# Optimization experiments

Measured on AMD Instinct MI355X. Metric: run time of the kernel, lower is better.

The kernel has to match this reference:

```python
import jax, jax.numpy as jnp
import numpy as np

B, N, DIM, DD = 32, 4096, 512, 512
SCALE = DD ** -0.5


def setup_inputs() -> dict:
    key = jax.random.key(0)
    ks = jax.random.split(key, 7)
    return {
        "x": jax.random.normal(ks[0], (B, N, DIM), dtype=jnp.float32),
        "Wq": jax.random.normal(ks[1], (DIM, DD), dtype=jnp.float32) * (DIM ** -0.5),
        "Wk": jax.random.normal(ks[2], (DIM, DD), dtype=jnp.float32) * (DIM ** -0.5),
        "Wv": jax.random.normal(ks[3], (DIM, DD), dtype=jnp.float32) * (DIM ** -0.5),
        "Wr": jax.random.normal(ks[4], (DD, DD), dtype=jnp.float32) * (DD ** -0.5),
        "alpha": jax.random.normal(ks[5], (DD,), dtype=jnp.float32),
        "beta": jax.random.normal(ks[6], (DD,), dtype=jnp.float32),
    }


def reference(x, Wq, Wk, Wv, Wr, alpha, beta):
    # projections: [b, n, d]
    q = jnp.einsum('bni,id->bnd', x, Wq)
    k = jnp.einsum('bni,id->bnd', x, Wk)
    v = jnp.einsum('bni,id->bnd', x, Wv)
    # additive attention over feature dim, pooled over sequence
    alpha_w = jax.nn.softmax(q * alpha * SCALE, axis=-1)
    global_query = jnp.sum(q * alpha_w, axis=1)            # [b, d]
    p = global_query[:, None, :] * k                        # [b, n, d]
    beta_w = jax.nn.softmax(p * beta * SCALE, axis=-1)
    global_key = jnp.sum(p * beta_w, axis=1)                # [b, d]
    kv = global_key[:, None, :] * v                         # [b, n, d]
    out = jnp.einsum('bnd,de->bne', kv, Wr) + q
    return out
```

## Files before the change

kernel.cpp:

```cpp
#include <hip/hip_runtime.h>


typedef __attribute__((ext_vector_type(8))) short short8;
typedef __attribute__((ext_vector_type(4))) float floatx4;
typedef unsigned short u16;
typedef unsigned int u32;

#define SEQ 4096
#define BATCH 32
#define NQKV 1536
#define FSCALE 0.044194173824159216f

__device__ __forceinline__ u16 f2bf(float f) {
  u32 u = __float_as_uint(f);
  u += 0x7fffu + ((u >> 16) & 1u);
  return (u16)(u >> 16);
}
__device__ __forceinline__ float bf2f(u16 h) { return __uint_as_float((u32)h << 16); }

__device__ __forceinline__ void g2l16(const void* g, void* l) {
  __builtin_amdgcn_global_load_lds(
      (const __attribute__((address_space(1))) void*)g,
      (__attribute__((address_space(3))) void*)l, 16, 0, 0);
}

__global__ __launch_bounds__(256) void convert_x(const float* __restrict__ x,
                                                 u16* __restrict__ xb) {
  size_t i = ((size_t)blockIdx.x * 256 + threadIdx.x) * 8;
  float4 f0 = *(const float4*)(x + i);
  float4 f1 = *(const float4*)(x + i + 4);
  short8 s;
  s[0] = (short)f2bf(f0.x); s[1] = (short)f2bf(f0.y);
  s[2] = (short)f2bf(f0.z); s[3] = (short)f2bf(f0.w);
  s[4] = (short)f2bf(f1.x); s[5] = (short)f2bf(f1.y);
  s[6] = (short)f2bf(f1.z); s[7] = (short)f2bf(f1.w);
  *(short8*)(xb + i) = s;
}

__global__ void prep_w(const float* __restrict__ Wq, const float* __restrict__ Wk,
                       const float* __restrict__ Wv, u16* __restrict__ Wt) {
  int n = blockIdx.x;
  const float* W = (n < 512) ? Wq : ((n < 1024) ? Wk : Wv);
  int col = n & 511;
  for (int kk = threadIdx.x; kk < 512; kk += 256)
    Wt[(size_t)n * 512 + kk] = f2bf(W[(size_t)kk * 512 + col]);
}

__global__ __launch_bounds__(256) void gemm_qkv(const u16* __restrict__ xb,
                                                const u16* __restrict__ Wt,
                                                u16* __restrict__ qkv) {
  __shared__ u16 sA[128 * 32];
  __shared__ u16 sB[128 * 32];
  const int tid = threadIdx.x;
  const int lane = tid & 63, wv = tid >> 6;
  const int row0 = blockIdx.y * 128;
  const int col0 = blockIdx.x * 128;
  const int wm = (wv >> 1) * 64, wn = (wv & 1) * 64;

  floatx4 acc[4][4] = {};
  const int ln = lane & 15;
  const int quad = (lane >> 4);
  const int b_row = (lane >> 2);
  const int b_kq = (lane & 3) * 8;

  for (int kt = 0; kt < 16; ++kt) {
    const int k0 = kt * 32;
    __syncthreads();
#pragma unroll
    for (int c = 0; c < 2; ++c) {
      int chunk = wv * 2 + c;
      int r = chunk * 16 + b_row;
      g2l16(xb + (size_t)(row0 + r) * 512 + k0 + b_kq, sA + chunk * 512 + lane * 8);
      g2l16(Wt + (size_t)(col0 + r) * 512 + k0 + b_kq, sB + chunk * 512 + lane * 8);
    }
    __syncthreads();

    short8 a[4], b[4];
#pragma unroll
    for (int i = 0; i < 4; ++i)
      a[i] = *(const short8*)&sA[(wm + i * 16 + ln) * 32 + quad * 8];
#pragma unroll
    for (int j = 0; j < 4; ++j)
      b[j] = *(const short8*)&sB[(wn + j * 16 + ln) * 32 + quad * 8];
#pragma unroll
    for (int i = 0; i < 4; ++i)
#pragma unroll
      for (int j = 0; j < 4; ++j)
        acc[i][j] = __builtin_amdgcn_mfma_f32_16x16x32_bf16(a[i], b[j], acc[i][j], 0, 0, 0);
  }

#pragma unroll
  for (int i = 0; i < 4; ++i) {
#pragma unroll
    for (int r = 0; r < 4; ++r) {
      int grow = row0 + wm + i * 16 + quad * 4 + r;
      size_t base = (size_t)grow * NQKV + col0 + wn + ln;
#pragma unroll
      for (int j = 0; j < 4; ++j)
        qkv[base + j * 16] = f2bf(acc[i][j][r]);
    }
  }
}

__global__ __launch_bounds__(256) void pool_alpha(const u16* __restrict__ qkv,
                                                  const float* __restrict__ alpha,
                                                  float* __restrict__ gq) {
  const int b = blockIdx.y;
  const int lane = threadIdx.x & 63, wv = threadIdx.x >> 6;
  const int slot = blockIdx.x * 4 + wv;
  float a8[8], acc8[8];
#pragma unroll
  for (int j = 0; j < 8; ++j) {
    a8[j] = alpha[lane * 8 + j] * FSCALE;
    acc8[j] = 0.f;
  }
  for (int i = 0; i < 64; ++i) {
    int row = slot * 64 + i;
    const u16* qr = qkv + (size_t)(b * SEQ + row) * NQKV + lane * 8;
    short8 s = *(const short8*)qr;
    float q[8], t[8];
    float m = -1e30f;
#pragma unroll
    for (int j = 0; j < 8; ++j) {
      q[j] = bf2f((u16)s[j]);
      t[j] = q[j] * a8[j];
      m = fmaxf(m, t[j]);
    }
#pragma unroll
    for (int off = 32; off >= 1; off >>= 1) m = fmaxf(m, __shfl_xor(m, off));
    float sum = 0.f;
    float e[8];
#pragma unroll
    for (int j = 0; j < 8; ++j) {
      e[j] = __expf(t[j] - m);
      sum += e[j];
    }
#pragma unroll
    for (int off = 32; off >= 1; off >>= 1) sum += __shfl_xor(sum, off);
    float inv = 1.f / sum;
#pragma unroll
    for (int j = 0; j < 8; ++j) acc8[j] += q[j] * e[j] * inv;
  }
#pragma unroll
  for (int j = 0; j < 8; ++j) atomicAdd(&gq[b * 512 + lane * 8 + j], acc8[j]);
}

__global__ __launch_bounds__(256) void pool_beta(const u16* __restrict__ qkv,
                                                 const float* __restrict__ beta,
                                                 const float* __restrict__ gq,
                                                 float* __restrict__ gk) {
  const int b = blockIdx.y;
  const int lane = threadIdx.x & 63, wv = threadIdx.x >> 6;
  const int slot = blockIdx.x * 4 + wv;
  float b8[8], g8[8], acc8[8];
#pragma unroll
  for (int j = 0; j < 8; ++j) {
    b8[j] = beta[lane * 8 + j] * FSCALE;
    g8[j] = gq[b * 512 + lane * 8 + j];
    acc8[j] = 0.f;
  }
  for (int i = 0; i < 64; ++i) {
    int row = slot * 64 + i;
    const u16* kr = qkv + (size_t)(b * SEQ + row) * NQKV + 512 + lane * 8;
    short8 s = *(const short8*)kr;
    float p[8], t[8];
    float m = -1e30f;
#pragma unroll
    for (int j = 0; j < 8; ++j) {
      p[j] = g8[j] * bf2f((u16)s[j]);
      t[j] = p[j] * b8[j];
      m = fmaxf(m, t[j]);
    }
#pragma unroll
    for (int off = 32; off >= 1; off >>= 1) m = fmaxf(m, __shfl_xor(m, off));
    float sum = 0.f;
    float e[8];
#pragma unroll
    for (int j = 0; j < 8; ++j) {
      e[j] = __expf(t[j] - m);
      sum += e[j];
    }
#pragma unroll
    for (int off = 32; off >= 1; off >>= 1) sum += __shfl_xor(sum, off);
    float inv = 1.f / sum;
#pragma unroll
    for (int j = 0; j < 8; ++j) acc8[j] += p[j] * e[j] * inv;
  }
#pragma unroll
  for (int j = 0; j < 8; ++j) atomicAdd(&gk[b * 512 + lane * 8 + j], acc8[j]);
}

__global__ void build_wrs(const float* __restrict__ Wr, const float* __restrict__ gk,
                          u16* __restrict__ Wrs) {
  int e = blockIdx.x, b = blockIdx.y;
  const float* g = gk + b * 512;
  u16* o = Wrs + ((size_t)b * 512 + e) * 512;
  for (int d = threadIdx.x; d < 512; d += 256)
    o[d] = f2bf(g[d] * Wr[(size_t)d * 512 + e]);
}

__global__ __launch_bounds__(256) void gemm_out(const u16* __restrict__ qkv,
                                                const u16* __restrict__ Wrs,
                                                float* __restrict__ out) {
  __shared__ u16 sA[128 * 32];
  __shared__ u16 sB[128 * 32];
  const int tid = threadIdx.x;
  const int lane = tid & 63, wv = tid >> 6;
  const int b = blockIdx.z;
  const int row0 = blockIdx.y * 128;
  const int col0 = blockIdx.x * 128;
  const int wm = (wv >> 1) * 64, wn = (wv & 1) * 64;

  floatx4 acc[4][4] = {};
  const int ln = lane & 15;
  const int quad = (lane >> 4);
  const int b_row = (lane >> 2);
  const int b_kq = (lane & 3) * 8;

  const u16* vbase = qkv + (size_t)b * SEQ * NQKV + 1024;
  const u16* wbase = Wrs + (size_t)b * 512 * 512;

  for (int kt = 0; kt < 16; ++kt) {
    const int k0 = kt * 32;
    __syncthreads();
#pragma unroll
    for (int c = 0; c < 2; ++c) {
      int chunk = wv * 2 + c;
      int r = chunk * 16 + b_row;
      g2l16(vbase + (size_t)(row0 + r) * NQKV + k0 + b_kq, sA + chunk * 512 + lane * 8);
      g2l16(wbase + (size_t)(col0 + r) * 512 + k0 + b_kq, sB + chunk * 512 + lane * 8);
    }
    __syncthreads();

    short8 a[4], bb[4];
#pragma unroll
    for (int i = 0; i < 4; ++i)
      a[i] = *(const short8*)&sA[(wm + i * 16 + ln) * 32 + quad * 8];
#pragma unroll
    for (int j = 0; j < 4; ++j)
      bb[j] = *(const short8*)&sB[(wn + j * 16 + ln) * 32 + quad * 8];
#pragma unroll
    for (int i = 0; i < 4; ++i)
#pragma unroll
      for (int j = 0; j < 4; ++j)
        acc[i][j] = __builtin_amdgcn_mfma_f32_16x16x32_bf16(a[i], bb[j], acc[i][j], 0, 0, 0);
  }

#pragma unroll
  for (int i = 0; i < 4; ++i) {
#pragma unroll
    for (int r = 0; r < 4; ++r) {
      int grow = row0 + wm + i * 16 + quad * 4 + r;
      size_t qrow = (size_t)(b * SEQ + grow) * NQKV;
      size_t orow = (size_t)(b * SEQ + grow) * 512;
#pragma unroll
      for (int j = 0; j < 4; ++j) {
        int gcol = col0 + wn + ln + j * 16;
        float qv = bf2f(qkv[qrow + gcol]);
        out[orow + gcol] = acc[i][j][r] + qv;
      }
    }
  }
}

extern "C" void kernel_launch(void* const* d_in, const int* in_sizes, int n_in,
                              void* d_out, int out_size, void* d_ws, size_t ws_size,
                              hipStream_t stream) {
  const float* x = (const float*)d_in[0];
  const float* Wq = (const float*)d_in[1];
  const float* Wk = (const float*)d_in[2];
  const float* Wv = (const float*)d_in[3];
  const float* Wr = (const float*)d_in[4];
  const float* alpha = (const float*)d_in[5];
  const float* beta = (const float*)d_in[6];
  float* out = (float*)d_out;

  char* ws = (char*)d_ws;
  u16* qkv = (u16*)ws;
  u16* Wt = (u16*)(ws + 402653184ull);
  u16* Wrs = (u16*)(ws + 402653184ull + 1572864ull);
  float* gq = (float*)(ws + 402653184ull + 1572864ull + 16777216ull);
  float* gk = gq + 16384;

  u16* xb = (u16*)d_out;

  hipMemsetAsync(gq, 0, 131072, stream);
  convert_x<<<32768, 256, 0, stream>>>(x, xb);
  prep_w<<<1536, 256, 0, stream>>>(Wq, Wk, Wv, Wt);
  gemm_qkv<<<dim3(12, 1024), 256, 0, stream>>>(xb, Wt, qkv);
  pool_alpha<<<dim3(16, BATCH), 256, 0, stream>>>(qkv, alpha, gq);
  pool_beta<<<dim3(16, BATCH), 256, 0, stream>>>(qkv, beta, gq, gk);
  build_wrs<<<dim3(512, BATCH), 256, 0, stream>>>(Wr, gk, Wrs);
  gemm_out<<<dim3(4, 32, BATCH), 256, 0, stream>>>(qkv, Wrs, out);
}
```

Measured before the change: 1.163 ms.

## Fold V projection, gk scaling, Wr and Q residual into per-batch output weight

Instead of computing V and then multiplying by a gk-scaled Wr, the output is rewritten as x times a per-batch fused matrix Wv·diag(gk)·Wr + Wq. That matrix is built with a small batched GEMM, and the final GEMM then reads x directly. This drops the V columns from the big projection GEMM and removes the separate residual read of q in the epilogue. It also adds a grouped block-index swizzle to the large GEMMs for cache locality. In exchange, Wq is now rounded to bf16 inside the fused weight, which changes numerics slightly, and the residual q is recomputed through the fused weight rather than reused.

```diff
diff --git a/kernel.cpp b/kernel.cpp
--- a/kernel.cpp
+++ b/kernel.cpp
@@ -8,7 +8,7 @@
 
 #define SEQ 4096
 #define BATCH 32
-#define NQKV 1536
+#define NQK 1024
 #define FSCALE 0.044194173824159216f
 
 __device__ __forceinline__ u16 f2bf(float f) {
@@ -38,40 +38,44 @@
 }
 
 __global__ void prep_w(const float* __restrict__ Wq, const float* __restrict__ Wk,
-                       const float* __restrict__ Wv, u16* __restrict__ Wt) {
+                       const float* __restrict__ Wr, u16* __restrict__ Wt,
+                       u16* __restrict__ Wrt) {
   int n = blockIdx.x;
-  const float* W = (n < 512) ? Wq : ((n < 1024) ? Wk : Wv);
-  int col = n & 511;
-  for (int kk = threadIdx.x; kk < 512; kk += 256)
-    Wt[(size_t)n * 512 + kk] = f2bf(W[(size_t)kk * 512 + col]);
-}
-
-__global__ __launch_bounds__(256) void gemm_qkv(const u16* __restrict__ xb,
-                                                const u16* __restrict__ Wt,
-                                                u16* __restrict__ qkv) {
-  __shared__ u16 sA[128 * 32];
-  __shared__ u16 sB[128 * 32];
+  if (n < 1024) {
+    const float* W = (n < 512) ? Wq : Wk;
+    int col = n & 511;
+    for (int kk = threadIdx.x; kk < 512; kk += 256)
+      Wt[(size_t)n * 512 + kk] = f2bf(W[(size_t)kk * 512 + col]);
+  } else {
+    int e = n - 1024;
+    for (int d = threadIdx.x; d < 512; d += 256)
+      Wrt[(size_t)e * 512 + d] = f2bf(Wr[(size_t)d * 512 + e]);
+  }
+}
+
+template <int LDA, int LDB, int KTILES>
+__device__ __forceinline__ void gemm_core(const u16* __restrict__ A,
+                                          const u16* __restrict__ B,
+                                          int row0, int col0,
+                                          u16* sA, u16* sB,
+                                          floatx4 (&acc)[4][4]) {
   const int tid = threadIdx.x;
   const int lane = tid & 63, wv = tid >> 6;
-  const int row0 = blockIdx.y * 128;
-  const int col0 = blockIdx.x * 128;
   const int wm = (wv >> 1) * 64, wn = (wv & 1) * 64;
-
-  floatx4 acc[4][4] = {};
   const int ln = lane & 15;
-  const int quad = (lane >> 4);
-  const int b_row = (lane >> 2);
+  const int quad = lane >> 4;
+  const int b_row = lane >> 2;
   const int b_kq = (lane & 3) * 8;
 
-  for (int kt = 0; kt < 16; ++kt) {
+  for (int kt = 0; kt < KTILES; ++kt) {
     const int k0 = kt * 32;
     __syncthreads();
 #pragma unroll
     for (int c = 0; c < 2; ++c) {
       int chunk = wv * 2 + c;
       int r = chunk * 16 + b_row;
-      g2l16(xb + (size_t)(row0 + r) * 512 + k0 + b_kq, sA + chunk * 512 + lane * 8);
-      g2l16(Wt + (size_t)(col0 + r) * 512 + k0 + b_kq, sB + chunk * 512 + lane * 8);
+      g2l16(A + (size_t)(row0 + r) * LDA + k0 + b_kq, sA + chunk * 512 + lane * 8);
+      g2l16(B + (size_t)(col0 + r) * LDB + k0 + b_kq, sB + chunk * 512 + lane * 8);
     }
     __syncthreads();
 
@@ -88,21 +92,37 @@
       for (int j = 0; j < 4; ++j)
         acc[i][j] = __builtin_amdgcn_mfma_f32_16x16x32_bf16(a[i], b[j], acc[i][j], 0, 0, 0);
   }
-
+}
+
+__global__ __launch_bounds__(256) void gemm_qk(const u16* __restrict__ xb,
+                                               const u16* __restrict__ Wt,
+                                               u16* __restrict__ qk) {
+  __shared__ u16 sA[128 * 32];
+  __shared__ u16 sB[128 * 32];
+  int bid = blockIdx.y * 8 + blockIdx.x;
+  int swz = (bid & 7) * 1024 + (bid >> 3);
+  const int row0 = (swz >> 3) * 128;
+  const int col0 = (swz & 7) * 128;
+
+  floatx4 acc[4][4] = {};
+  gemm_core<512, 512, 16>(xb, Wt, row0, col0, sA, sB, acc);
+
+  const int lane = threadIdx.x & 63, wv = threadIdx.x >> 6;
+  const int wm = (wv >> 1) * 64, wn = (wv & 1) * 64;
+  const int ln = lane & 15, quad = lane >> 4;
 #pragma unroll
   for (int i = 0; i < 4; ++i) {
 #pragma unroll
     for (int r = 0; r < 4; ++r) {
       int grow = row0 + wm + i * 16 + quad * 4 + r;
-      size_t base = (size_t)grow * NQKV + col0 + wn + ln;
-#pragma unroll
-      for (int j = 0; j < 4; ++j)
-        qkv[base + j * 16] = f2bf(acc[i][j][r]);
-    }
-  }
-}
-
-__global__ __launch_bounds__(256) void pool_alpha(const u16* __restrict__ qkv,
+      size_t base = (size_t)grow * NQK + col0 + wn + ln;
+#pragma unroll
+      for (int j = 0; j < 4; ++j) qk[base + j * 16] = f2bf(acc[i][j][r]);
+    }
+  }
+}
+
+__global__ __launch_bounds__(256) void pool_alpha(const u16* __restrict__ qk,
                                                   const float* __restrict__ alpha,
                                                   float* __restrict__ gq) {
   const int b = blockIdx.y;
@@ -116,7 +136,7 @@
   }
   for (int i = 0; i < 64; ++i) {
     int row = slot * 64 + i;
-    const u16* qr = qkv + (size_t)(b * SEQ + row) * NQKV + lane * 8;
+    const u16* qr = qk + (size_t)(b * SEQ + row) * NQK + lane * 8;
     short8 s = *(const short8*)qr;
     float q[8], t[8];
     float m = -1e30f;
@@ -145,7 +165,7 @@
   for (int j = 0; j < 8; ++j) atomicAdd(&gq[b * 512 + lane * 8 + j], acc8[j]);
 }
 
-__global__ __launch_bounds__(256) void pool_beta(const u16* __restrict__ qkv,
+__global__ __launch_bounds__(256) void pool_beta(const u16* __restrict__ qk,
                                                  const float* __restrict__ beta,
                                                  const float* __restrict__ gq,
                                                  float* __restrict__ gk) {
@@ -161,7 +181,7 @@
   }
   for (int i = 0; i < 64; ++i) {
     int row = slot * 64 + i;
-    const u16* kr = qkv + (size_t)(b * SEQ + row) * NQKV + 512 + lane * 8;
+    const u16* kr = qk + (size_t)(b * SEQ + row) * NQK + 512 + lane * 8;
     short8 s = *(const short8*)kr;
     float p[8], t[8];
     float m = -1e30f;
@@ -190,74 +210,76 @@
   for (int j = 0; j < 8; ++j) atomicAdd(&gk[b * 512 + lane * 8 + j], acc8[j]);
 }
 
-__global__ void build_wrs(const float* __restrict__ Wr, const float* __restrict__ gk,
-                          u16* __restrict__ Wrs) {
-  int e = blockIdx.x, b = blockIdx.y;
-  const float* g = gk + b * 512;
-  u16* o = Wrs + ((size_t)b * 512 + e) * 512;
-  for (int d = threadIdx.x; d < 512; d += 256)
-    o[d] = f2bf(g[d] * Wr[(size_t)d * 512 + e]);
-}
-
-__global__ __launch_bounds__(256) void gemm_out(const u16* __restrict__ qkv,
-                                                const u16* __restrict__ Wrs,
-                                                float* __restrict__ out) {
+__global__ void build_vgk(const float* __restrict__ Wv, const float* __restrict__ gk,
+                          u16* __restrict__ Vgk) {
+  int i = blockIdx.x, b = blockIdx.y;
+  const float* gr = gk + b * 512;
+  const float* wr = Wv + (size_t)i * 512;
+  u16* o = Vgk + ((size_t)b * 512 + i) * 512;
+  for (int d = threadIdx.x; d < 512; d += 256) o[d] = f2bf(wr[d] * gr[d]);
+}
+
+__global__ __launch_bounds__(256) void gemm_wfin(const u16* __restrict__ Wrt,
+                                                 const u16* __restrict__ Vgk,
+                                                 const float* __restrict__ Wq,
+                                                 u16* __restrict__ Wfin) {
   __shared__ u16 sA[128 * 32];
   __shared__ u16 sB[128 * 32];
-  const int tid = threadIdx.x;
-  const int lane = tid & 63, wv = tid >> 6;
   const int b = blockIdx.z;
   const int row0 = blockIdx.y * 128;
   const int col0 = blockIdx.x * 128;
+  const u16* Bb = Vgk + (size_t)b * 512 * 512;
+  u16* Cb = Wfin + (size_t)b * 512 * 512;
+
+  floatx4 acc[4][4] = {};
+  gemm_core<512, 512, 16>(Wrt, Bb, row0, col0, sA, sB, acc);
+
+  const int lane = threadIdx.x & 63, wv = threadIdx.x >> 6;
   const int wm = (wv >> 1) * 64, wn = (wv & 1) * 64;
-
-  floatx4 acc[4][4] = {};
-  const int ln = lane & 15;
-  const int quad = (lane >> 4);
-  const int b_row = (lane >> 2);
-  const int b_kq = (lane & 3) * 8;
-
-  const u16* vbase = qkv + (size_t)b * SEQ * NQKV + 1024;
-  const u16* wbase = Wrs + (size_t)b * 512 * 512;
-
-  for (int kt = 0; kt < 16; ++kt) {
-    const int k0 = kt * 32;
-    __syncthreads();
-#pragma unroll
-    for (int c = 0; c < 2; ++c) {
-      int chunk = wv * 2 + c;
-      int r = chunk * 16 + b_row;
-      g2l16(vbase + (size_t)(row0 + r) * NQKV + k0 + b_kq, sA + chunk * 512 + lane * 8);
-      g2l16(wbase + (size_t)(col0 + r) * 512 + k0 + b_kq, sB + chunk * 512 + lane * 8);
-    }
-    __syncthreads();
-
-    short8 a[4], bb[4];
-#pragma unroll
-    for (int i = 0; i < 4; ++i)
-      a[i] = *(const short8*)&sA[(wm + i * 16 + ln) * 32 + quad * 8];
-#pragma unroll
-    for (int j = 0; j < 4; ++j)
-      bb[j] = *(const short8*)&sB[(wn + j * 16 + ln) * 32 + quad * 8];
-#pragma unroll
-    for (int i = 0; i < 4; ++i)
-#pragma unroll
-      for (int j = 0; j < 4; ++j)
-        acc[i][j] = __builtin_amdgcn_mfma_f32_16x16x32_bf16(a[i], bb[j], acc[i][j], 0, 0, 0);
-  }
-
+  const int ln = lane & 15, quad = lane >> 4;
 #pragma unroll
   for (int i = 0; i < 4; ++i) {
 #pragma unroll
     for (int r = 0; r < 4; ++r) {
       int grow = row0 + wm + i * 16 + quad * 4 + r;
-      size_t qrow = (size_t)(b * SEQ + grow) * NQKV;
-      size_t orow = (size_t)(b * SEQ + grow) * 512;
 #pragma unroll
       for (int j = 0; j < 4; ++j) {
         int gcol = col0 + wn + ln + j * 16;
-        float qv = bf2f(qkv[qrow + gcol]);
-        out[orow + gcol] = acc[i][j][r] + qv;
+        Cb[(size_t)grow * 512 + gcol] = f2bf(acc[i][j][r] + Wq[(size_t)gcol * 512 + grow]);
+      }
+    }
+  }
+}
+
+__global__ __launch_bounds__(256) void gemm_final(const u16* __restrict__ xb,
+                                                  const u16* __restrict__ Wfin,
+                                                  float* __restrict__ out) {
+  __shared__ u16 sA[128 * 32];
+  __shared__ u16 sB[128 * 32];
+  const int b = blockIdx.z;
+  int bid = blockIdx.y * 4 + blockIdx.x;
+  int swz = (bid & 7) * 16 + (bid >> 3);
+  const int row0 = (swz >> 2) * 128;
+  const int col0 = (swz & 3) * 128;
+  const u16* Ab = xb + (size_t)b * SEQ * 512;
+  const u16* Bb = Wfin + (size_t)b * 512 * 512;
+
+  floatx4 acc[4][4] = {};
+  gemm_core<512, 512, 16>(Ab, Bb, row0, col0, sA, sB, acc);
+
+  const int lane = threadIdx.x & 63, wv = threadIdx.x >> 6;
+  const int wm = (wv >> 1) * 64, wn = (wv & 1) * 64;
+  const int ln = lane & 15, quad = lane >> 4;
+#pragma unroll
+  for (int i = 0; i < 4; ++i) {
+#pragma unroll
+    for (int r = 0; r < 4; ++r) {
+      int grow = row0 + wm + i * 16 + quad * 4 + r;
+      size_t orow = ((size_t)b * SEQ + grow) * 512;
+#pragma unroll
+      for (int j = 0; j < 4; ++j) {
+        int gcol = col0 + wn + ln + j * 16;
+        out[orow + gcol] = acc[i][j][r];
       }
     }
   }
@@ -276,20 +298,22 @@
   float* out = (float*)d_out;
 
   char* ws = (char*)d_ws;
-  u16* qkv = (u16*)ws;
+  u16* xb = (u16*)ws;
+  u16* qk = (u16*)(ws + 134217728ull);
+  u16* Vgk = (u16*)(ws + 134217728ull);
+  u16* Wfin = (u16*)(ws + 151994944ull);
   u16* Wt = (u16*)(ws + 402653184ull);
-  u16* Wrs = (u16*)(ws + 402653184ull + 1572864ull);
-  float* gq = (float*)(ws + 402653184ull + 1572864ull + 16777216ull);
+  u16* Wrt = (u16*)(ws + 403701760ull);
+  float* gq = (float*)(ws + 404226048ull);
   float* gk = gq + 16384;
-
-  u16* xb = (u16*)d_out;
 
   hipMemsetAsync(gq, 0, 131072, stream);
   convert_x<<<32768, 256, 0, stream>>>(x, xb);
-  prep_w<<<1536, 256, 0, stream>>>(Wq, Wk, Wv, Wt);
-  gemm_qkv<<<dim3(12, 1024), 256, 0, stream>>>(xb, Wt, qkv);
-  pool_alpha<<<dim3(16, BATCH), 256, 0, stream>>>(qkv, alpha, gq);
-  pool_beta<<<dim3(16, BATCH), 256, 0, stream>>>(qkv, beta, gq, gk);
-  build_wrs<<<dim3(512, BATCH), 256, 0, stream>>>(Wr, gk, Wrs);
-  gemm_out<<<dim3(4, 32, BATCH), 256, 0, stream>>>(qkv, Wrs, out);
-}
+  prep_w<<<1536, 256, 0, stream>>>(Wq, Wk, Wr, Wt, Wrt);
+  gemm_qk<<<dim3(8, 1024), 256, 0, stream>>>(xb, Wt, qk);
+  pool_alpha<<<dim3(16, BATCH), 256, 0, stream>>>(qk, alpha, gq);
+  pool_beta<<<dim3(16, BATCH), 256, 0, stream>>>(qk, beta, gq, gk);
+  build_vgk<<<dim3(512, BATCH), 256, 0, stream>>>(Wv, gk, Vgk);
+  gemm_wfin<<<dim3(4, 4, BATCH), 256, 0, stream>>>(Wrt, Vgk, Wq, Wfin);
+  gemm_final<<<dim3(4, 32, BATCH), 256, 0, stream>>>(xb, Wfin, out);
+}
```

New measurement: 1.042 ms. -10.4%, faster.
